# Kernel optimization log

Hardware: AMD Instinct MI355X
Metric: run time of the kernel (lower is better)

Reference implementation:

```python
import jax, jax.numpy as jnp
import numpy as np

EPS = 1e-5

def layer_norm(x, w, b):
    mu = x.mean(-1, keepdims=True)
    var = x.var(-1, keepdims=True)
    return (x - mu) / jnp.sqrt(var + EPS) * w + b

def s5_forward(u, Lambda_re, Lambda_im, B_re, B_im, C_re, C_im, D, log_step):
    # u: [B, L, H]; diagonal S5 SSM with P complex states, ZOH discretization.
    Lam = (Lambda_re + 1j * Lambda_im).astype(jnp.complex64)          # [P]
    dt = jnp.exp(log_step).astype(jnp.complex64)                       # [P]
    Lam_bar = jnp.exp(Lam * dt)                                        # [P]
    Bc = (B_re + 1j * B_im).astype(jnp.complex64)                      # [P, H]
    B_bar = ((Lam_bar - 1.0) / Lam)[:, None] * Bc                      # [P, H]
    Bu = jnp.einsum('blh,ph->blp', u.astype(jnp.complex64), B_bar)     # [B, L, P]
    A = jnp.broadcast_to(Lam_bar, Bu.shape)                            # [B, L, P]

    def binop(e1, e2):
        a1, b1 = e1
        a2, b2 = e2
        return (a2 * a1, a2 * b1 + b2)

    _, xs = jax.lax.associative_scan(binop, (A, Bu), axis=1)           # [B, L, P]
    Cc = (C_re + 1j * C_im).astype(jnp.complex64)                      # [H, P]
    y = 2.0 * jnp.einsum('blp,hp->blh', xs, Cc).real + D * u           # [B, L, H]
    return y

def setup_inputs() -> dict:
    key = jax.random.key(0)
    ks = jax.random.split(key, 12)
    B, L, H, P = 4, 4096, 512, 512
    x = jax.random.normal(ks[0], (B, L, H), jnp.float32)
    # SSM params (HiPPO-like flavor: negative real part, spread imaginary part)
    Lambda_re = -(0.5 * jax.random.uniform(ks[1], (P,), jnp.float32) + 0.1)
    Lambda_im = jnp.pi * jnp.arange(P, dtype=jnp.float32)
    B_re = jax.random.normal(ks[2], (P, H), jnp.float32) / np.sqrt(2.0 * H)
    B_im = jax.random.normal(ks[3], (P, H), jnp.float32) / np.sqrt(2.0 * H)
    C_re = jax.random.normal(ks[4], (H, P), jnp.float32) / np.sqrt(P)
    C_im = jax.random.normal(ks[5], (H, P), jnp.float32) / np.sqrt(P)
    D = jax.random.normal(ks[6], (H,), jnp.float32)
    log_step = jax.random.uniform(ks[7], (P,), jnp.float32,
                                  minval=np.log(1e-3), maxval=np.log(1e-1))
    ln1_w = jnp.ones((H,), jnp.float32); ln1_b = jnp.zeros((H,), jnp.float32)
    ln2_w = jnp.ones((H,), jnp.float32); ln2_b = jnp.zeros((H,), jnp.float32)
    W_enc = jax.random.normal(ks[8], (2 * H, H), jnp.float32) / np.sqrt(H)
    W_dec = jax.random.normal(ks[9], (H, H), jnp.float32) / np.sqrt(H)
    return {"x": x, "ln1_w": ln1_w, "ln1_b": ln1_b,
            "Lambda_re": Lambda_re, "Lambda_im": Lambda_im,
            "B_re": B_re, "B_im": B_im, "C_re": C_re, "C_im": C_im,
            "D": D, "log_step": log_step,
            "ln2_w": ln2_w, "ln2_b": ln2_b, "W_enc": W_enc, "W_dec": W_dec}

def reference(x, ln1_w, ln1_b, Lambda_re, Lambda_im, B_re, B_im, C_re, C_im,
              D, log_step, ln2_w, ln2_b, W_enc, W_dec):
    fx = layer_norm(x, ln1_w, ln1_b)
    res = fx
    u = s5_forward(fx, Lambda_re, Lambda_im, B_re, B_im, C_re, C_im, D, log_step)
    h = jax.nn.gelu(u, approximate=False) + res  # eval mode: dropout = identity
    fx2 = layer_norm(h, ln2_w, ln2_b)
    e = fx2 @ W_enc.T                              # [B, L, 2H]
    a, g = jnp.split(e, 2, axis=-1)
    ff = a * jax.nn.gelu(g, approximate=False)     # GEGLU
    out = ff @ W_dec.T + fx2
    return out
```

## Files before the change

kernel.cpp:

```cpp
#include <hip/hip_runtime.h>
#include <math.h>

#define Bz 4
#define Lz 4096
#define Hz 512
#define Pz 512
#define Nz (Bz*Lz)
#define CL 64
#define NC (Lz/CL)
#define CS (Bz*NC*Pz)
#define EPSf 1e-5f

typedef unsigned short u16;
typedef unsigned int   u32;
typedef __attribute__((ext_vector_type(8))) short bf16x8;
typedef __attribute__((ext_vector_type(8))) short short8v;
typedef __attribute__((ext_vector_type(4))) float f32x4;

__device__ __forceinline__ float gelu_exact(float x){
    return 0.5f * x * (1.0f + erff(x * 0.70710678118654752f));
}
__device__ __forceinline__ u16 f2b(float f){
    union { float f; u32 u; } v; v.f = f;
    u32 u = v.u;
    u32 r = (u + 0x7FFFu + ((u >> 16) & 1u)) >> 16;
    return (u16)r;
}
__device__ __forceinline__ float b2f(u16 h){
    union { u32 u; float f; } v; v.u = ((u32)h) << 16; return v.f;
}

__device__ __forceinline__ void gload_lds16(const u16* g, u16* l){
    __builtin_amdgcn_global_load_lds(
        (const __attribute__((address_space(1))) void*)g,
        (__attribute__((address_space(3))) void*)l, 16, 0, 0);
}

__device__ __forceinline__ void load8(const float* p, float* v){
    f32x4 a = *(const f32x4*)p, c = *(const f32x4*)(p+4);
    #pragma unroll
    for (int j=0;j<4;++j){ v[j]=a[j]; v[4+j]=c[j]; }
}
__device__ __forceinline__ void load8(const u16* p, float* v){
    short8v s = *(const short8v*)p;
    #pragma unroll
    for (int j=0;j<8;++j) v[j] = b2f((u16)s[j]);
}

__global__ void setup_kernel(const float* __restrict__ Lre, const float* __restrict__ Lim,
                             const float* __restrict__ log_step,
                             float* __restrict__ prm){
    int p = blockIdx.x*blockDim.x + threadIdx.x;
    if (p >= Pz) return;
    float lr = Lre[p], li = Lim[p];
    float dt = expf(log_step[p]);
    float ar = lr*dt, ai = li*dt;
    float e = expf(ar);
    float Abr = e*cosf(ai), Abi = e*sinf(ai);
    prm[p]        = Abr;
    prm[Pz + p]   = Abi;
    float nr = Abr - 1.0f, ni = Abi;
    float d2 = lr*lr + li*li;
    prm[2*Pz + p] = (nr*lr + ni*li)/d2;
    prm[3*Pz + p] = (ni*lr - nr*li)/d2;
    float arC = ar*(float)CL, aiC = ai*(float)CL;
    float eC = expf(arC);
    prm[4*Pz + p] = eC*cosf(aiC);
    prm[5*Pz + p] = eC*sinf(aiC);
}

__global__ __launch_bounds__(256) void cvt_all(const float* __restrict__ B_re,
                                               const float* __restrict__ B_im,
                                               const float* __restrict__ C_re,
                                               const float* __restrict__ C_im,
                                               const float* __restrict__ W_enc,
                                               const float* __restrict__ W_dec,
                                               u16* __restrict__ Bcat,
                                               u16* __restrict__ Ccat,
                                               u16* __restrict__ Wenc,
                                               u16* __restrict__ Wdec){
    const int Q = 512*512;
    int i = blockIdx.x*256 + threadIdx.x;
    if (i < Q){ int p=i>>9, h=i&511; Bcat[(size_t)(2*p)*512 + h]   = f2b(B_re[i]); return; }
    i -= Q;
    if (i < Q){ int p=i>>9, h=i&511; Bcat[(size_t)(2*p+1)*512 + h] = f2b(B_im[i]); return; }
    i -= Q;
    if (i < Q){
        int h = i >> 9, p = i & 511;
        Ccat[(size_t)h*1024 + 2*p]     = f2b(C_re[i]);
        Ccat[(size_t)h*1024 + 2*p + 1] = f2b(-C_im[i]);
        return;
    }
    i -= Q;
    if (i < 2*Q){ Wenc[i] = f2b(W_enc[i]); return; }
    i -= 2*Q;
    Wdec[i] = f2b(W_dec[i]);
}

template<typename T>
__global__ __launch_bounds__(256) void ln_kernel(const T* __restrict__ in,
                                                 const float* __restrict__ w,
                                                 const float* __restrict__ b,
                                                 u16* __restrict__ ob){
    int row = blockIdx.x*4 + (threadIdx.x >> 6);
    int l = threadIdx.x & 63;
    float v[8];
    load8(in + (size_t)row*Hz + l*8, v);
    float s = 0.f, q = 0.f;
    #pragma unroll
    for (int j=0;j<8;++j){ s += v[j]; q += v[j]*v[j]; }
    #pragma unroll
    for (int o=32;o;o>>=1){ s += __shfl_xor(s,o); q += __shfl_xor(q,o); }
    float mu = s * (1.0f/512.0f);
    float rs = rsqrtf(q * (1.0f/512.0f) - mu*mu + EPSf);
    short8v o8;
    #pragma unroll
    for (int j=0;j<8;++j){
        int m = l*8 + j;
        o8[j] = (short)f2b((v[j]-mu)*rs*w[m] + b[m]);
    }
    *(short8v*)&ob[(size_t)row*Hz + l*8] = o8;
}

#define EB16 0
#define EY   1
#define ERES 2

__device__ __forceinline__ void stage128(const u16* __restrict__ src, int ld,
                                         int grow0, int kt, u16* lds){
    int lane = threadIdx.x & 63;
    int w    = threadIdx.x >> 6;
    #pragma unroll
    for (int q = 0; q < 4; ++q){
        int c = w + q*4;
        int r = c*8 + (lane >> 3);
        int colE = 8*((lane & 7) ^ ((lane >> 3) & 7));
        const u16* g = src + (size_t)(grow0 + r)*ld + kt + colE;
        gload_lds16(g, lds + c*512);
    }
}

template<int K, int EPI>
__global__ __launch_bounds__(256, 2)
void gemm2p(const u16* __restrict__ A, const u16* __restrict__ Bw, int M,
            u16* __restrict__ outB,
            const u16* __restrict__ fxB,
            const float* __restrict__ Dv,
            const u16* __restrict__ resB,
            float* __restrict__ outF)
{
    constexpr int NT = K/64;
    __shared__ u16 AL[2][128*64];
    __shared__ u16 BL[2][128*64];

    int nx = gridDim.x, ny = gridDim.y;
    int nwg = nx*ny;
    int lid = blockIdx.x + blockIdx.y*nx;
    int cpx = nwg >> 3;
    int gdx = (lid & 7)*cpx + (lid >> 3);
    int n0 = (gdx / ny) * 128;
    int m0 = (gdx % ny) * 128;

    int l = threadIdx.x & 63;
    int w = threadIdx.x >> 6;
    int lrow  = l & 15;
    int lcol0 = ((l >> 4)*8) ^ ((l & 7) << 3);
    int lcol1 = lcol0 ^ 32;
    int colw  = w*32;

    f32x4 acc[8][2];
    #pragma unroll
    for (int i=0;i<8;++i){ acc[i][0]=(f32x4)(0.f); acc[i][1]=(f32x4)(0.f); }

    stage128(A,  K, n0, 0, &AL[0][0]);
    stage128(Bw, K, m0, 0, &BL[0][0]);
    __syncthreads();

    for (int T=0; T<NT; ++T){
        int buf = T & 1, nb = buf ^ 1;
        if (T+1 < NT){
            int ktn = (T+1)*64;
            stage128(A,  K, n0, ktn, &AL[nb][0]);
            stage128(Bw, K, m0, ktn, &BL[nb][0]);
        }
        const u16* Ab = &AL[buf][0];
        const u16* Bb = &BL[buf][0];
        bf16x8 bfr[2][2];
        #pragma unroll
        for (int fn=0; fn<2; ++fn){
            bfr[0][fn] = *(const bf16x8*)&Bb[(colw + fn*16 + lrow)*64 + lcol0];
            bfr[1][fn] = *(const bf16x8*)&Bb[(colw + fn*16 + lrow)*64 + lcol1];
        }
        #pragma unroll
        for (int f=0; f<8; ++f){
            bf16x8 a0 = *(const bf16x8*)&Ab[(f*16 + lrow)*64 + lcol0];
            bf16x8 a1 = *(const bf16x8*)&Ab[(f*16 + lrow)*64 + lcol1];
            #pragma unroll
            for (int fn=0; fn<2; ++fn){
                acc[f][fn] = __builtin_amdgcn_mfma_f32_16x16x32_bf16(a0, bfr[0][fn], acc[f][fn], 0,0,0);
                acc[f][fn] = __builtin_amdgcn_mfma_f32_16x16x32_bf16(a1, bfr[1][fn], acc[f][fn], 0,0,0);
            }
        }
        __syncthreads();
    }

    int er = (l >> 4) * 4;
    int ec = l & 15;
    #pragma unroll
    for (int fm=0; fm<8; ++fm)
        #pragma unroll
        for (int fn=0; fn<2; ++fn)
            #pragma unroll
            for (int q=0; q<4; ++q){
                int n = n0 + fm*16 + er + q;
                int m = m0 + colw + fn*16 + ec;
                float v = acc[fm][fn][q];
                if (EPI == EB16){
                    outB[(size_t)n*M + m] = f2b(v);
                } else if (EPI == EY){
                    size_t idx = (size_t)n*Hz + m;
                    float fxv = b2f(fxB[idx]);
                    float y = 2.0f*v + Dv[m]*fxv;
                    outB[idx] = f2b(gelu_exact(y) + fxv);
                } else {
                    size_t idx = (size_t)n*Hz + m;
                    outF[idx] = v + b2f(resB[idx]);
                }
            }
}

__global__ __launch_bounds__(256, 2)
void gemm1_scan(const u16* __restrict__ A, const u16* __restrict__ Bw,
                u16* __restrict__ outB,
                const float* __restrict__ prm,
                float* __restrict__ ERe, float* __restrict__ EIm)
{
    constexpr int K = 512, NT = K/64;
    __shared__ u16 AL[2][128*64];
    __shared__ u16 BL[2][128*64];

    int nx = gridDim.x, ny = gridDim.y;
    int nwg = nx*ny;
    int lid = blockIdx.x + blockIdx.y*nx;
    int cpx = nwg >> 3;
    int gdx = (lid & 7)*cpx + (lid >> 3);
    int n0 = (gdx / ny) * 128;
    int m0 = (gdx % ny) * 128;

    int l = threadIdx.x & 63;
    int w = threadIdx.x >> 6;
    int lrow  = l & 15;
    int lcol0 = ((l >> 4)*8) ^ ((l & 7) << 3);
    int lcol1 = lcol0 ^ 32;
    int colw  = w*32;

    f32x4 acc[8][2];
    #pragma unroll
    for (int i=0;i<8;++i){ acc[i][0]=(f32x4)(0.f); acc[i][1]=(f32x4)(0.f); }

    stage128(A,  K, n0, 0, &AL[0][0]);
    stage128(Bw, K, m0, 0, &BL[0][0]);
    __syncthreads();

    for (int T=0; T<NT; ++T){
        int buf = T & 1, nb = buf ^ 1;
        if (T+1 < NT){
            int ktn = (T+1)*64;
            stage128(A,  K, n0, ktn, &AL[nb][0]);
            stage128(Bw, K, m0, ktn, &BL[nb][0]);
        }
        const u16* Ab = &AL[buf][0];
        const u16* Bb = &BL[buf][0];
        bf16x8 bfr[2][2];
        #pragma unroll
        for (int fn=0; fn<2; ++fn){
            bfr[0][fn] = *(const bf16x8*)&Bb[(colw + fn*16 + lrow)*64 + lcol0];
            bfr[1][fn] = *(const bf16x8*)&Bb[(colw + fn*16 + lrow)*64 + lcol1];
        }
        #pragma unroll
        for (int f=0; f<8; ++f){
            bf16x8 a0 = *(const bf16x8*)&Ab[(f*16 + lrow)*64 + lcol0];
            bf16x8 a1 = *(const bf16x8*)&Ab[(f*16 + lrow)*64 + lcol1];
            #pragma unroll
            for (int fn=0; fn<2; ++fn){
                acc[f][fn] = __builtin_amdgcn_mfma_f32_16x16x32_bf16(a0, bfr[0][fn], acc[f][fn], 0,0,0);
                acc[f][fn] = __builtin_amdgcn_mfma_f32_16x16x32_bf16(a1, bfr[1][fn], acc[f][fn], 0,0,0);
            }
        }
        __syncthreads();
    }

    u16* gt = (u16*)AL;
    int er = (l >> 4) * 4;
    int ec = l & 15;
    #pragma unroll
    for (int fm=0; fm<8; ++fm)
        #pragma unroll
        for (int fn=0; fn<2; ++fn)
            #pragma unroll
            for (int q=0; q<4; ++q){
                int rr = fm*16 + er + q;
                int cc = colw + fn*16 + ec;
                u16 hv = f2b(acc[fm][fn][q]);
                outB[(size_t)(n0 + rr)*1024 + (m0 + cc)] = hv;
                gt[rr*128 + cc] = hv;
            }
    __syncthreads();

    int tid = threadIdx.x;
    if (tid < 128){
        int p = tid & 63, h = tid >> 6;
        int P = (m0 >> 1) + p;
        int b = n0 >> 12;
        int c = ((n0 & 4095) >> 6) + h;
        float Ar = prm[P], Ai = prm[Pz+P];
        float fre = prm[2*Pz+P], fim = prm[3*Pz+P];
        float xr = 0.f, xi = 0.f;
        int base = h*64*128 + 2*p;
        #pragma unroll 8
        for (int r = 0; r < 64; ++r){
            u32 v = *(const u32*)&gt[base + r*128];
            float gr = b2f((u16)(v & 0xffff));
            float gi = b2f((u16)(v >> 16));
            float br = fre*gr - fim*gi;
            float bi = fre*gi + fim*gr;
            float nr2 = Ar*xr - Ai*xi + br;
            float ni2 = Ar*xi + Ai*xr + bi;
            xr = nr2; xi = ni2;
        }
        size_t ci = ((size_t)(b*NC + c))*Pz + P;
        ERe[ci] = xr; EIm[ci] = xi;
    }
}

__device__ __forceinline__ void stageWglu(const u16* __restrict__ src, int m0,
                                          int kt, u16* lds){
    int lane = threadIdx.x & 63;
    int w    = threadIdx.x >> 6;
    #pragma unroll
    for (int q = 0; q < 4; ++q){
        int c = w + q*4;
        int r = c*8 + (lane >> 3);
        int rb = r >> 4;
        int grow = (rb & 1) ? (512 + m0 + ((rb>>1)<<4) + (r & 15))
                            : (      m0 + ((rb>>1)<<4) + (r & 15));
        int colE = 8*((lane & 7) ^ ((lane >> 3) & 7));
        gload_lds16(src + (size_t)grow*512 + kt + colE, lds + c*512);
    }
}

__global__ __launch_bounds__(256, 2)
void gemm3glu(const u16* __restrict__ A, const u16* __restrict__ Wenc,
              u16* __restrict__ outB)
{
    constexpr int K = 512, NT = K/64;
    __shared__ u16 AL[2][128*64];
    __shared__ u16 BL[2][128*64];

    int nx = gridDim.x, ny = gridDim.y;
    int nwg = nx*ny;
    int lid = blockIdx.x + blockIdx.y*nx;
    int cpx = nwg >> 3;
    int gdx = (lid & 7)*cpx + (lid >> 3);
    int n0 = (gdx / ny) * 128;
    int m0 = (gdx % ny) * 64;

    int l = threadIdx.x & 63;
    int w = threadIdx.x >> 6;
    int lrow  = l & 15;
    int lcol0 = ((l >> 4)*8) ^ ((l & 7) << 3);
    int lcol1 = lcol0 ^ 32;
    int colw  = w*32;

    f32x4 acc[8][2];
    #pragma unroll
    for (int i=0;i<8;++i){ acc[i][0]=(f32x4)(0.f); acc[i][1]=(f32x4)(0.f); }

    stage128(A, K, n0, 0, &AL[0][0]);
    stageWglu(Wenc, m0, 0, &BL[0][0]);
    __syncthreads();

    for (int T=0; T<NT; ++T){
        int buf = T & 1, nb = buf ^ 1;
        if (T+1 < NT){
            int ktn = (T+1)*64;
            stage128(A, K, n0, ktn, &AL[nb][0]);
            stageWglu(Wenc, m0, ktn, &BL[nb][0]);
        }
        const u16* Ab = &AL[buf][0];
        const u16* Bb = &BL[buf][0];
        bf16x8 bfr[2][2];
        #pragma unroll
        for (int fn=0; fn<2; ++fn){
            bfr[0][fn] = *(const bf16x8*)&Bb[(colw + fn*16 + lrow)*64 + lcol0];
            bfr[1][fn] = *(const bf16x8*)&Bb[(colw + fn*16 + lrow)*64 + lcol1];
        }
        #pragma unroll
        for (int f=0; f<8; ++f){
            bf16x8 a0 = *(const bf16x8*)&Ab[(f*16 + lrow)*64 + lcol0];
            bf16x8 a1 = *(const bf16x8*)&Ab[(f*16 + lrow)*64 + lcol1];
            #pragma unroll
            for (int fn=0; fn<2; ++fn){
                acc[f][fn] = __builtin_amdgcn_mfma_f32_16x16x32_bf16(a0, bfr[0][fn], acc[f][fn], 0,0,0);
                acc[f][fn] = __builtin_amdgcn_mfma_f32_16x16x32_bf16(a1, bfr[1][fn], acc[f][fn], 0,0,0);
            }
        }
        __syncthreads();
    }

    int er = (l >> 4) * 4;
    int ec = l & 15;
    int col = m0 + w*16 + ec;
    #pragma unroll
    for (int fm=0; fm<8; ++fm)
        #pragma unroll
        for (int q=0; q<4; ++q){
            int n = n0 + fm*16 + er + q;
            float ffv = acc[fm][0][q] * gelu_exact(acc[fm][1][q]);
            outB[(size_t)n*Hz + col] = f2b(ffv);
        }
}

__global__ __launch_bounds__(256) void scan_combine(const float* __restrict__ ERe,
                                                    const float* __restrict__ EIm,
                                                    const float* __restrict__ prm,
                                                    float* __restrict__ SinRe,
                                                    float* __restrict__ SinIm){
    int gt = blockIdx.x*256 + threadIdx.x;
    int b = gt / Pz, p = gt % Pz;
    float Ar = prm[4*Pz+p], Ai = prm[5*Pz+p];
    float Sr = 0.f, Si = 0.f;
    for (int c = 0; c < NC; ++c) {
        size_t idx = ((size_t)(b*NC + c))*Pz + p;
        SinRe[idx] = Sr; SinIm[idx] = Si;
        float er = ERe[idx], ei = EIm[idx];
        float nr = Ar*Sr - Ai*Si + er;
        float ni = Ar*Si + Ai*Sr + ei;
        Sr = nr; Si = ni;
    }
}

__global__ __launch_bounds__(64) void scan_phase2(u16* __restrict__ g,
                                                  const float* __restrict__ prm,
                                                  const float* __restrict__ SinRe,
                                                  const float* __restrict__ SinIm){
    int t = blockIdx.x;
    int ph = t & 1; t >>= 1;
    int c  = t % NC;
    int b  = t / NC;
    int p0 = ph*256 + threadIdx.x*4;
    int cb = 2*p0;
    size_t base = ((size_t)(b*Lz + c*CL))*1024;
    size_t ci = ((size_t)(b*NC + c))*Pz + p0;
    float Ar[4], Ai[4], fr[4], fi[4], xr[4], xi[4];
    f32x4 sr4 = *(const f32x4*)&SinRe[ci];
    f32x4 si4 = *(const f32x4*)&SinIm[ci];
    #pragma unroll
    for (int j=0;j<4;++j){
        Ar[j]=prm[p0+j]; Ai[j]=prm[Pz+p0+j];
        fr[j]=prm[2*Pz+p0+j]; fi[j]=prm[3*Pz+p0+j];
        xr[j]=sr4[j]; xi[j]=si4[j];
    }
    for (int ll=0; ll<CL; ++ll){
        short8v v8 = *(const short8v*)&g[base + cb];
        short8v o8;
        #pragma unroll
        for (int j=0;j<4;++j){
            float gr = b2f((u16)v8[2*j]), gi = b2f((u16)v8[2*j+1]);
            float br = fr[j]*gr - fi[j]*gi;
            float bi = fr[j]*gi + fi[j]*gr;
            float nr = Ar[j]*xr[j] - Ai[j]*xi[j] + br;
            float ni = Ar[j]*xi[j] + Ai[j]*xr[j] + bi;
            xr[j]=nr; xi[j]=ni;
            o8[2*j]   = (short)f2b(nr);
            o8[2*j+1] = (short)f2b(ni);
        }
        *(short8v*)&g[base + cb] = o8;
        base += 1024;
    }
}

extern "C" void kernel_launch(void* const* d_in, const int* in_sizes, int n_in,
                              void* d_out, int out_size, void* d_ws, size_t ws_size,
                              hipStream_t stream) {
    const float* x        = (const float*)d_in[0];
    const float* ln1_w    = (const float*)d_in[1];
    const float* ln1_b    = (const float*)d_in[2];
    const float* Lre      = (const float*)d_in[3];
    const float* Lim      = (const float*)d_in[4];
    const float* B_re     = (const float*)d_in[5];
    const float* B_im     = (const float*)d_in[6];
    const float* C_re     = (const float*)d_in[7];
    const float* C_im     = (const float*)d_in[8];
    const float* Dv       = (const float*)d_in[9];
    const float* log_step = (const float*)d_in[10];
    const float* ln2_w    = (const float*)d_in[11];
    const float* ln2_b    = (const float*)d_in[12];
    const float* W_enc    = (const float*)d_in[13];
    const float* W_dec    = (const float*)d_in[14];
    float* out = (float*)d_out;

    const size_t NH = (size_t)Nz*Hz;
    char* W = (char*)d_ws;
    u16*   fxb  = (u16*)  (W);
    u16*   g    = (u16*)  (W + NH*2);
    u16*   hb   = (u16*)  (W + NH*6);
    u16*   fx2b = (u16*)  (W + NH*8);
    float* ERe  = (float*)(W + NH*10);
    float* EIm  = ERe + CS;
    float* SinRe= EIm + CS;
    float* SinIm= SinRe + CS;
    float* prm  = SinIm + CS;
    u16*   Bcat = (u16*)(prm + 6*Pz);
    u16*   Ccat = Bcat + 1024*512;
    u16*   Wenc = Ccat + 512*1024;
    u16*   Wdec = Wenc + 1024*512;

    setup_kernel<<<dim3(2), dim3(256), 0, stream>>>(Lre, Lim, log_step, prm);

    cvt_all<<<dim3(6*1024), dim3(256), 0, stream>>>(B_re, B_im, C_re, C_im, W_enc, W_dec,
                                                    Bcat, Ccat, Wenc, Wdec);

    ln_kernel<float><<<dim3(Nz/4), dim3(256), 0, stream>>>(x, ln1_w, ln1_b, fxb);

    gemm1_scan<<<dim3(Nz/128, 1024/128), dim3(256), 0, stream>>>(
        fxb, Bcat, g, prm, ERe, EIm);

    scan_combine<<<dim3((Bz*Pz)/256), dim3(256), 0, stream>>>(ERe, EIm, prm, SinRe, SinIm);
    scan_phase2<<<dim3(Bz*NC*2), dim3(64), 0, stream>>>(g, prm, SinRe, SinIm);

    gemm2p<1024,EY><<<dim3(Nz/128, 512/128), dim3(256), 0, stream>>>(
        g, Ccat, 512, hb, fxb, Dv, nullptr, nullptr);

    ln_kernel<u16><<<dim3(Nz/4), dim3(256), 0, stream>>>(hb, ln2_w, ln2_b, fx2b);

    gemm3glu<<<dim3(Nz/128, 8), dim3(256), 0, stream>>>(fx2b, Wenc, fxb);

    gemm2p<512,ERES><<<dim3(Nz/128, 512/128), dim3(256), 0, stream>>>(
        fxb, Wdec, 512, nullptr, nullptr, nullptr, fx2b, out);
}
```

Measured before the change: 185.6 us.

## Replace LDS-staged GEMMs with direct global-to-register MFMA loads in 2x2 wave tiles

All four GEMM kernels stop staging A and B tiles into LDS via global_load_lds double buffering. Each wave now loads its bf16 fragments straight from global memory into registers and computes a 64x64 sub-tile in a 2x2 wave arrangement. Launch bounds rise to 4 blocks per CU. This removes LDS traffic and barriers, but each operand row is loaded separately by two waves, so more redundant global/L2 reads occur and there is no explicit prefetch to hide latency.

Measured after the change: 322.9 us. +73.9%, slower.

```diff
diff --git a/kernel.cpp b/kernel.cpp
--- a/kernel.cpp
+++ b/kernel.cpp
@@ -28,12 +28,6 @@
 }
 __device__ __forceinline__ float b2f(u16 h){
     union { u32 u; float f; } v; v.u = ((u32)h) << 16; return v.f;
-}
-
-__device__ __forceinline__ void gload_lds16(const u16* g, u16* l){
-    __builtin_amdgcn_global_load_lds(
-        (const __attribute__((address_space(1))) void*)g,
-        (__attribute__((address_space(3))) void*)l, 16, 0, 0);
 }
 
 __device__ __forceinline__ void load8(const float* p, float* v){
@@ -126,33 +120,15 @@
 #define EY   1
 #define ERES 2
 
-__device__ __forceinline__ void stage128(const u16* __restrict__ src, int ld,
-                                         int grow0, int kt, u16* lds){
-    int lane = threadIdx.x & 63;
-    int w    = threadIdx.x >> 6;
-    #pragma unroll
-    for (int q = 0; q < 4; ++q){
-        int c = w + q*4;
-        int r = c*8 + (lane >> 3);
-        int colE = 8*((lane & 7) ^ ((lane >> 3) & 7));
-        const u16* g = src + (size_t)(grow0 + r)*ld + kt + colE;
-        gload_lds16(g, lds + c*512);
-    }
-}
-
 template<int K, int EPI>
-__global__ __launch_bounds__(256, 2)
-void gemm2p(const u16* __restrict__ A, const u16* __restrict__ Bw, int M,
-            u16* __restrict__ outB,
-            const u16* __restrict__ fxB,
-            const float* __restrict__ Dv,
-            const u16* __restrict__ resB,
-            float* __restrict__ outF)
+__global__ __launch_bounds__(256, 4)
+void gemmr(const u16* __restrict__ A, const u16* __restrict__ Bw, int M,
+           u16* __restrict__ outB,
+           const u16* __restrict__ fxB,
+           const float* __restrict__ Dv,
+           const u16* __restrict__ resB,
+           float* __restrict__ outF)
 {
-    constexpr int NT = K/64;
-    __shared__ u16 AL[2][128*64];
-    __shared__ u16 BL[2][128*64];
-
     int nx = gridDim.x, ny = gridDim.y;
     int nwg = nx*ny;
     int lid = blockIdx.x + blockIdx.y*nx;
@@ -163,57 +139,43 @@
 
     int l = threadIdx.x & 63;
     int w = threadIdx.x >> 6;
-    int lrow  = l & 15;
-    int lcol0 = ((l >> 4)*8) ^ ((l & 7) << 3);
-    int lcol1 = lcol0 ^ 32;
-    int colw  = w*32;
-
-    f32x4 acc[8][2];
-    #pragma unroll
-    for (int i=0;i<8;++i){ acc[i][0]=(f32x4)(0.f); acc[i][1]=(f32x4)(0.f); }
-
-    stage128(A,  K, n0, 0, &AL[0][0]);
-    stage128(Bw, K, m0, 0, &BL[0][0]);
-    __syncthreads();
-
-    for (int T=0; T<NT; ++T){
-        int buf = T & 1, nb = buf ^ 1;
-        if (T+1 < NT){
-            int ktn = (T+1)*64;
-            stage128(A,  K, n0, ktn, &AL[nb][0]);
-            stage128(Bw, K, m0, ktn, &BL[nb][0]);
-        }
-        const u16* Ab = &AL[buf][0];
-        const u16* Bb = &BL[buf][0];
-        bf16x8 bfr[2][2];
-        #pragma unroll
-        for (int fn=0; fn<2; ++fn){
-            bfr[0][fn] = *(const bf16x8*)&Bb[(colw + fn*16 + lrow)*64 + lcol0];
-            bfr[1][fn] = *(const bf16x8*)&Bb[(colw + fn*16 + lrow)*64 + lcol1];
-        }
-        #pragma unroll
-        for (int f=0; f<8; ++f){
-            bf16x8 a0 = *(const bf16x8*)&Ab[(f*16 + lrow)*64 + lcol0];
-            bf16x8 a1 = *(const bf16x8*)&Ab[(f*16 + lrow)*64 + lcol1];
-            #pragma unroll
-            for (int fn=0; fn<2; ++fn){
-                acc[f][fn] = __builtin_amdgcn_mfma_f32_16x16x32_bf16(a0, bfr[0][fn], acc[f][fn], 0,0,0);
-                acc[f][fn] = __builtin_amdgcn_mfma_f32_16x16x32_bf16(a1, bfr[1][fn], acc[f][fn], 0,0,0);
-            }
-        }
-        __syncthreads();
+    int wr = w >> 1, wc = w & 1;
+    int rbase = wr*64, cbase = wc*64;
+    int lr15 = l & 15;
+    int koff = (l >> 4) * 8;
+
+    const u16* Ap = A  + (size_t)(n0 + rbase + lr15)*K + koff;
+    const u16* Bp = Bw + (size_t)(m0 + cbase + lr15)*K + koff;
+
+    f32x4 acc[4][4];
+    #pragma unroll
+    for (int i=0;i<4;++i)
+        #pragma unroll
+        for (int j=0;j<4;++j) acc[i][j] = (f32x4)(0.f);
+
+    for (int k0 = 0; k0 < K; k0 += 32){
+        bf16x8 af[4], bf[4];
+        #pragma unroll
+        for (int i=0;i<4;++i) af[i] = *(const bf16x8*)(Ap + (size_t)(16*i)*K + k0);
+        #pragma unroll
+        for (int j=0;j<4;++j) bf[j] = *(const bf16x8*)(Bp + (size_t)(16*j)*K + k0);
+        #pragma unroll
+        for (int i=0;i<4;++i)
+            #pragma unroll
+            for (int j=0;j<4;++j)
+                acc[i][j] = __builtin_amdgcn_mfma_f32_16x16x32_bf16(af[i], bf[j], acc[i][j], 0,0,0);
     }
 
     int er = (l >> 4) * 4;
     int ec = l & 15;
     #pragma unroll
-    for (int fm=0; fm<8; ++fm)
-        #pragma unroll
-        for (int fn=0; fn<2; ++fn)
+    for (int fm=0; fm<4; ++fm)
+        #pragma unroll
+        for (int fn=0; fn<4; ++fn)
             #pragma unroll
             for (int q=0; q<4; ++q){
-                int n = n0 + fm*16 + er + q;
-                int m = m0 + colw + fn*16 + ec;
+                int n = n0 + rbase + fm*16 + er + q;
+                int m = m0 + cbase + fn*16 + ec;
                 float v = acc[fm][fn][q];
                 if (EPI == EB16){
                     outB[(size_t)n*M + m] = f2b(v);
@@ -229,15 +191,14 @@
             }
 }
 
-__global__ __launch_bounds__(256, 2)
-void gemm1_scan(const u16* __restrict__ A, const u16* __restrict__ Bw,
-                u16* __restrict__ outB,
-                const float* __restrict__ prm,
-                float* __restrict__ ERe, float* __restrict__ EIm)
+__global__ __launch_bounds__(256, 4)
+void gemm1r_scan(const u16* __restrict__ A, const u16* __restrict__ Bw,
+                 u16* __restrict__ outB,
+                 const float* __restrict__ prm,
+                 float* __restrict__ ERe, float* __restrict__ EIm)
 {
-    constexpr int K = 512, NT = K/64;
-    __shared__ u16 AL[2][128*64];
-    __shared__ u16 BL[2][128*64];
+    constexpr int K = 512;
+    __shared__ u16 gt[128*128];
 
     int nx = gridDim.x, ny = gridDim.y;
     int nwg = nx*ny;
@@ -249,58 +210,43 @@
 
     int l = threadIdx.x & 63;
     int w = threadIdx.x >> 6;
-    int lrow  = l & 15;
-    int lcol0 = ((l >> 4)*8) ^ ((l & 7) << 3);
-    int lcol1 = lcol0 ^ 32;
-    int colw  = w*32;
-
-    f32x4 acc[8][2];
-    #pragma unroll
-    for (int i=0;i<8;++i){ acc[i][0]=(f32x4)(0.f); acc[i][1]=(f32x4)(0.f); }
-
-    stage128(A,  K, n0, 0, &AL[0][0]);
-    stage128(Bw, K, m0, 0, &BL[0][0]);
-    __syncthreads();
-
-    for (int T=0; T<NT; ++T){
-        int buf = T & 1, nb = buf ^ 1;
-        if (T+1 < NT){
-            int ktn = (T+1)*64;
-            stage128(A,  K, n0, ktn, &AL[nb][0]);
-            stage128(Bw, K, m0, ktn, &BL[nb][0]);
-        }
-        const u16* Ab = &AL[buf][0];
-        const u16* Bb = &BL[buf][0];
-        bf16x8 bfr[2][2];
-        #pragma unroll
-        for (int fn=0; fn<2; ++fn){
-            bfr[0][fn] = *(const bf16x8*)&Bb[(colw + fn*16 + lrow)*64 + lcol0];
-            bfr[1][fn] = *(const bf16x8*)&Bb[(colw + fn*16 + lrow)*64 + lcol1];
-        }
-        #pragma unroll
-        for (int f=0; f<8; ++f){
-            bf16x8 a0 = *(const bf16x8*)&Ab[(f*16 + lrow)*64 + lcol0];
-            bf16x8 a1 = *(const bf16x8*)&Ab[(f*16 + lrow)*64 + lcol1];
-            #pragma unroll
-            for (int fn=0; fn<2; ++fn){
-                acc[f][fn] = __builtin_amdgcn_mfma_f32_16x16x32_bf16(a0, bfr[0][fn], acc[f][fn], 0,0,0);
-                acc[f][fn] = __builtin_amdgcn_mfma_f32_16x16x32_bf16(a1, bfr[1][fn], acc[f][fn], 0,0,0);
-            }
-        }
-        __syncthreads();
-    }
-
-    u16* gt = (u16*)AL;
+    int wr = w >> 1, wc = w & 1;
+    int rbase = wr*64, cbase = wc*64;
+    int lr15 = l & 15;
+    int koff = (l >> 4) * 8;
+
+    const u16* Ap = A  + (size_t)(n0 + rbase + lr15)*K + koff;
+    const u16* Bp = Bw + (size_t)(m0 + cbase + lr15)*K + koff;
+
+    f32x4 acc[4][4];
+    #pragma unroll
+    for (int i=0;i<4;++i)
+        #pragma unroll
+        for (int j=0;j<4;++j) acc[i][j] = (f32x4)(0.f);
+
+    for (int k0 = 0; k0 < K; k0 += 32){
+        bf16x8 af[4], bf[4];
+        #pragma unroll
+        for (int i=0;i<4;++i) af[i] = *(const bf16x8*)(Ap + (size_t)(16*i)*K + k0);
+        #pragma unroll
+        for (int j=0;j<4;++j) bf[j] = *(const bf16x8*)(Bp + (size_t)(16*j)*K + k0);
+        #pragma unroll
+        for (int i=0;i<4;++i)
+            #pragma unroll
+            for (int j=0;j<4;++j)
+                acc[i][j] = __builtin_amdgcn_mfma_f32_16x16x32_bf16(af[i], bf[j], acc[i][j], 0,0,0);
+    }
+
     int er = (l >> 4) * 4;
     int ec = l & 15;
     #pragma unroll
-    for (int fm=0; fm<8; ++fm)
-        #pragma unroll
-        for (int fn=0; fn<2; ++fn)
+    for (int fm=0; fm<4; ++fm)
+        #pragma unroll
+        for (int fn=0; fn<4; ++fn)
             #pragma unroll
             for (int q=0; q<4; ++q){
-                int rr = fm*16 + er + q;
-                int cc = colw + fn*16 + ec;
+                int rr = rbase + fm*16 + er + q;
+                int cc = cbase + fn*16 + ec;
                 u16 hv = f2b(acc[fm][fn][q]);
                 outB[(size_t)(n0 + rr)*1024 + (m0 + cc)] = hv;
                 gt[rr*128 + cc] = hv;
@@ -333,92 +279,67 @@
     }
 }
 
-__device__ __forceinline__ void stageWglu(const u16* __restrict__ src, int m0,
-                                          int kt, u16* lds){
-    int lane = threadIdx.x & 63;
-    int w    = threadIdx.x >> 6;
-    #pragma unroll
-    for (int q = 0; q < 4; ++q){
-        int c = w + q*4;
-        int r = c*8 + (lane >> 3);
-        int rb = r >> 4;
-        int grow = (rb & 1) ? (512 + m0 + ((rb>>1)<<4) + (r & 15))
-                            : (      m0 + ((rb>>1)<<4) + (r & 15));
-        int colE = 8*((lane & 7) ^ ((lane >> 3) & 7));
-        gload_lds16(src + (size_t)grow*512 + kt + colE, lds + c*512);
-    }
-}
-
-__global__ __launch_bounds__(256, 2)
-void gemm3glu(const u16* __restrict__ A, const u16* __restrict__ Wenc,
-              u16* __restrict__ outB)
+__global__ __launch_bounds__(256, 4)
+void gemm3r_glu(const u16* __restrict__ A, const u16* __restrict__ Wenc,
+                u16* __restrict__ outB)
 {
-    constexpr int K = 512, NT = K/64;
-    __shared__ u16 AL[2][128*64];
-    __shared__ u16 BL[2][128*64];
-
+    constexpr int K = 512;
     int nx = gridDim.x, ny = gridDim.y;
     int nwg = nx*ny;
     int lid = blockIdx.x + blockIdx.y*nx;
     int cpx = nwg >> 3;
     int gdx = (lid & 7)*cpx + (lid >> 3);
     int n0 = (gdx / ny) * 128;
-    int m0 = (gdx % ny) * 64;
+    int fb = (gdx % ny) * 64;
 
     int l = threadIdx.x & 63;
     int w = threadIdx.x >> 6;
-    int lrow  = l & 15;
-    int lcol0 = ((l >> 4)*8) ^ ((l & 7) << 3);
-    int lcol1 = lcol0 ^ 32;
-    int colw  = w*32;
-
-    f32x4 acc[8][2];
-    #pragma unroll
-    for (int i=0;i<8;++i){ acc[i][0]=(f32x4)(0.f); acc[i][1]=(f32x4)(0.f); }
-
-    stage128(A, K, n0, 0, &AL[0][0]);
-    stageWglu(Wenc, m0, 0, &BL[0][0]);
-    __syncthreads();
-
-    for (int T=0; T<NT; ++T){
-        int buf = T & 1, nb = buf ^ 1;
-        if (T+1 < NT){
-            int ktn = (T+1)*64;
-            stage128(A, K, n0, ktn, &AL[nb][0]);
-            stageWglu(Wenc, m0, ktn, &BL[nb][0]);
-        }
-        const u16* Ab = &AL[buf][0];
-        const u16* Bb = &BL[buf][0];
-        bf16x8 bfr[2][2];
-        #pragma unroll
-        for (int fn=0; fn<2; ++fn){
-            bfr[0][fn] = *(const bf16x8*)&Bb[(colw + fn*16 + lrow)*64 + lcol0];
-            bfr[1][fn] = *(const bf16x8*)&Bb[(colw + fn*16 + lrow)*64 + lcol1];
-        }
-        #pragma unroll
-        for (int f=0; f<8; ++f){
-            bf16x8 a0 = *(const bf16x8*)&Ab[(f*16 + lrow)*64 + lcol0];
-            bf16x8 a1 = *(const bf16x8*)&Ab[(f*16 + lrow)*64 + lcol1];
-            #pragma unroll
-            for (int fn=0; fn<2; ++fn){
-                acc[f][fn] = __builtin_amdgcn_mfma_f32_16x16x32_bf16(a0, bfr[0][fn], acc[f][fn], 0,0,0);
-                acc[f][fn] = __builtin_amdgcn_mfma_f32_16x16x32_bf16(a1, bfr[1][fn], acc[f][fn], 0,0,0);
-            }
-        }
-        __syncthreads();
+    int wr = w >> 1, wc = w & 1;
+    int rbase = wr*64;
+    int lr15 = l & 15;
+    int koff = (l >> 4) * 8;
+
+    const u16* Ap = A + (size_t)(n0 + rbase + lr15)*K + koff;
+    const u16* Bp[4];
+    #pragma unroll
+    for (int fn=0; fn<4; ++fn){
+        int gl = wc*4 + fn;
+        int row = ((gl & 1) ? 512 : 0) + fb + (gl >> 1)*16 + lr15;
+        Bp[fn] = Wenc + (size_t)row*K + koff;
+    }
+
+    f32x4 acc[4][4];
+    #pragma unroll
+    for (int i=0;i<4;++i)
+        #pragma unroll
+        for (int j=0;j<4;++j) acc[i][j] = (f32x4)(0.f);
+
+    for (int k0 = 0; k0 < K; k0 += 32){
+        bf16x8 af[4], bf[4];
+        #pragma unroll
+        for (int i=0;i<4;++i) af[i] = *(const bf16x8*)(Ap + (size_t)(16*i)*K + k0);
+        #pragma unroll
+        for (int j=0;j<4;++j) bf[j] = *(const bf16x8*)(Bp[j] + k0);
+        #pragma unroll
+        for (int i=0;i<4;++i)
+            #pragma unroll
+            for (int j=0;j<4;++j)
+                acc[i][j] = __builtin_amdgcn_mfma_f32_16x16x32_bf16(af[i], bf[j], acc[i][j], 0,0,0);
     }
 
     int er = (l >> 4) * 4;
     int ec = l & 15;
-    int col = m0 + w*16 + ec;
-    #pragma unroll
-    for (int fm=0; fm<8; ++fm)
-        #pragma unroll
-        for (int q=0; q<4; ++q){
-            int n = n0 + fm*16 + er + q;
-            float ffv = acc[fm][0][q] * gelu_exact(acc[fm][1][q]);
-            outB[(size_t)n*Hz + col] = f2b(ffv);
-        }
+    #pragma unroll
+    for (int fm=0; fm<4; ++fm)
+        #pragma unroll
+        for (int pr=0; pr<2; ++pr)
+            #pragma unroll
+            for (int q=0; q<4; ++q){
+                int n = n0 + rbase + fm*16 + er + q;
+                int col = fb + (wc*2 + pr)*16 + ec;
+                float ffv = acc[fm][2*pr][q] * gelu_exact(acc[fm][2*pr+1][q]);
+                outB[(size_t)n*Hz + col] = f2b(ffv);
+            }
 }
 
 __global__ __launch_bounds__(256) void scan_combine(const float* __restrict__ ERe,
@@ -523,19 +444,19 @@
 
     ln_kernel<float><<<dim3(Nz/4), dim3(256), 0, stream>>>(x, ln1_w, ln1_b, fxb);
 
-    gemm1_scan<<<dim3(Nz/128, 1024/128), dim3(256), 0, stream>>>(
+    gemm1r_scan<<<dim3(Nz/128, 1024/128), dim3(256), 0, stream>>>(
         fxb, Bcat, g, prm, ERe, EIm);
 
     scan_combine<<<dim3((Bz*Pz)/256), dim3(256), 0, stream>>>(ERe, EIm, prm, SinRe, SinIm);
     scan_phase2<<<dim3(Bz*NC*2), dim3(64), 0, stream>>>(g, prm, SinRe, SinIm);
 
-    gemm2p<1024,EY><<<dim3(Nz/128, 512/128), dim3(256), 0, stream>>>(
+    gemmr<1024,EY><<<dim3(Nz/128, 512/128), dim3(256), 0, stream>>>(
         g, Ccat, 512, hb, fxb, Dv, nullptr, nullptr);
 
     ln_kernel<u16><<<dim3(Nz/4), dim3(256), 0, stream>>>(hb, ln2_w, ln2_b, fx2b);
 
-    gemm3glu<<<dim3(Nz/128, 8), dim3(256), 0, stream>>>(fx2b, Wenc, fxb);
-
-    gemm2p<512,ERES><<<dim3(Nz/128, 512/128), dim3(256), 0, stream>>>(
+    gemm3r_glu<<<dim3(Nz/128, 8), dim3(256), 0, stream>>>(fx2b, Wenc, fxb);
+
+    gemmr<512,ERES><<<dim3(Nz/128, 512/128), dim3(256), 0, stream>>>(
         fxb, Wdec, 512, nullptr, nullptr, nullptr, fx2b, out);
 }
```
